# Performance work log

Hardware: AMD Instinct MI355X
Metric: run time of the kernel (lower is better)

Reference implementation:

```python
import jax, jax.numpy as jnp
import numpy as np

EPS = 1e-12  # torch F.normalize eps

def _l2norm(x):
    n = jnp.linalg.norm(x, axis=1, keepdims=True)
    return x / jnp.maximum(n, EPS)

def setup_inputs() -> dict:
    key = jax.random.key(0)
    kq, km = jax.random.split(key)
    queries = jax.random.normal(kq, (4096, 128), dtype=jnp.float32)
    memory = jax.random.normal(km, (100000, 128), dtype=jnp.float32)
    return {"queries": queries, "memory": memory, "k": 3}

def reference(queries, memory, k):
    q = _l2norm(queries)                      # [N, D]
    m = _l2norm(memory)                       # [M, D]
    sims = q @ m.T                            # [N, M]
    values, indices = jax.lax.top_k(sims, k)  # [N, k] each
    distances = 1.0 - values
    return distances, indices
```

## Files before the change

kernel.cpp:

```cpp
#include <hip/hip_runtime.h>
#include <hip/hip_bf16.h>

typedef unsigned short u16;
typedef unsigned int u32;
typedef unsigned long long u64;

#define N_Q 4096
#define N_M 100000
#define N_M_PAD 100096
#define DDIM 128
#define QTILE 256
#define MTILE 64
#define NCHUNK 32
#define NQT (N_Q / QTILE)
#define TOTAL_MT (N_M_PAD / MTILE)
#define TPC ((TOTAL_MT + NCHUNK - 1) / NCHUNK)
#define NCAND (NCHUNK * 2 * 3)

typedef short bf16x8 __attribute__((ext_vector_type(8)));
typedef float f32x4 __attribute__((ext_vector_type(4)));

static __device__ __forceinline__ u16 f2bf(float v) {
  union { float f; u32 u; } a; a.f = v;
  u32 r = a.u + 0x7fffu + ((a.u >> 16) & 1u);
  return (u16)(r >> 16);
}

static __device__ __forceinline__ void async_copy16(const u16* gp, u16* lp) {
  __builtin_amdgcn_global_load_lds(
      (const __attribute__((address_space(1))) u32*)gp,
      (__attribute__((address_space(3))) u32*)lp, 16, 0, 0);
}

static __device__ __forceinline__ int mbcnt64(u64 m) {
  return __builtin_amdgcn_mbcnt_hi((u32)(m >> 32),
                                   __builtin_amdgcn_mbcnt_lo((u32)m, 0));
}

__global__ __launch_bounds__(256) void knorm(const float* __restrict__ q, const float* __restrict__ m,
                                             u16* __restrict__ qn, u16* __restrict__ mn,
                                             float* __restrict__ qinv, float* __restrict__ minv) {
  const int lane = threadIdx.x & 63;
  const int l16 = lane & 15;
  const int sub = lane >> 4;
  const int wgl = blockIdx.x * 4 + (threadIdx.x >> 6);
  const int step = gridDim.x * 16;
  for (int row = wgl * 4 + sub; row < N_Q + N_M_PAD; row += step) {
    const float* src;
    u16* dst;
    int mr = 0;
    bool is_q = (row < N_Q);
    bool pad = false;
    if (is_q) {
      src = q + (size_t)row * DDIM;
      dst = qn + (size_t)row * DDIM;
    } else {
      mr = row - N_Q;
      pad = (mr >= N_M);
      src = m + (size_t)mr * DDIM;
      dst = mn + (size_t)mr * DDIM;
    }
    float4 a, b;
    if (pad) {
      a.x = a.y = a.z = a.w = 0.f;
      b = a;
    } else {
      a = ((const float4*)src)[l16];
      b = ((const float4*)src)[l16 + 16];
    }
    float s = a.x * a.x + a.y * a.y + a.z * a.z + a.w * a.w +
              b.x * b.x + b.y * b.y + b.z * b.z + b.w * b.w;
    #pragma unroll
    for (int off = 1; off < 16; off <<= 1) s += __shfl_xor(s, off, 64);
    float invn = 1.0f / fmaxf(sqrtf(s), 1e-12f);
    u32 p0 = (u32)f2bf(a.x * invn) | ((u32)f2bf(a.y * invn) << 16);
    u32 p1 = (u32)f2bf(a.z * invn) | ((u32)f2bf(a.w * invn) << 16);
    u32 p2 = (u32)f2bf(b.x * invn) | ((u32)f2bf(b.y * invn) << 16);
    u32 p3 = (u32)f2bf(b.z * invn) | ((u32)f2bf(b.w * invn) << 16);
    uint2 w0; w0.x = p0; w0.y = p1;
    uint2 w1; w1.x = p2; w1.y = p3;
    *(uint2*)&dst[l16 * 4] = w0;
    *(uint2*)&dst[64 + l16 * 4] = w1;
    if (l16 == 0) {
      if (is_q) qinv[row] = invn;
      else minv[mr] = pad ? 0.f : invn;
    }
  }
}

static __device__ __forceinline__ void stage2(const u16* __restrict__ mn, u16* dst,
                                              int t, const u32* goff, u32 loff0) {
  const u16* gbase = mn + (size_t)t * MTILE * DDIM;
  #pragma unroll
  for (int it = 0; it < 2; ++it)
    async_copy16(gbase + goff[it], dst + loff0 + (u32)(it * 64) * 8);
}

static __device__ __forceinline__ void tileWork(
    const u16* As, int tl, int wm, int quad, int l15,
    const bf16x8 (&bq)[4][4], float (&tv0)[4], float (&tv1)[4], float (&tv2)[4]) {
  f32x4 acc[2][4];
  __builtin_amdgcn_s_setprio(1);
  {
    int c = quad ^ l15;
    bf16x8 a0 = *(const bf16x8*)&As[((wm * 32 + l15) * 16 + c) * 8];
    bf16x8 a1 = *(const bf16x8*)&As[((wm * 32 + 16 + l15) * 16 + c) * 8];
    f32x4 z = {0.f, 0.f, 0.f, 0.f};
    #pragma unroll
    for (int ni = 0; ni < 4; ++ni) {
      acc[0][ni] = __builtin_amdgcn_mfma_f32_16x16x32_bf16(a0, bq[ni][0], z, 0, 0, 0);
      acc[1][ni] = __builtin_amdgcn_mfma_f32_16x16x32_bf16(a1, bq[ni][0], z, 0, 0, 0);
    }
  }
  #pragma unroll
  for (int s = 1; s < 4; ++s) {
    int c = (s * 4 + quad) ^ l15;
    bf16x8 a0 = *(const bf16x8*)&As[((wm * 32 + l15) * 16 + c) * 8];
    bf16x8 a1 = *(const bf16x8*)&As[((wm * 32 + 16 + l15) * 16 + c) * 8];
    #pragma unroll
    for (int ni = 0; ni < 4; ++ni) {
      acc[0][ni] = __builtin_amdgcn_mfma_f32_16x16x32_bf16(a0, bq[ni][s], acc[0][ni], 0, 0, 0);
      acc[1][ni] = __builtin_amdgcn_mfma_f32_16x16x32_bf16(a1, bq[ni][s], acc[1][ni], 0, 0, 0);
    }
  }
  __builtin_amdgcn_s_setprio(0);
  const u32 code = ((u32)tl << 2) | (u32)quad;
  #pragma unroll
  for (int ni = 0; ni < 4; ++ni) {
    f32x4 x0 = acc[0][ni], x1 = acc[1][ni];
    float M = fmaxf(fmaxf(fmaxf(x0[0], x0[1]), fmaxf(x0[2], x0[3])),
                    fmaxf(fmaxf(x1[0], x1[1]), fmaxf(x1[2], x1[3])));
    float pk = __uint_as_float((__float_as_uint(M) & 0xFFFFFE00u) | code);
    tv2[ni] = __builtin_amdgcn_fmed3f(tv1[ni], tv2[ni], pk);
    tv1[ni] = __builtin_amdgcn_fmed3f(tv0[ni], tv1[ni], pk);
    tv0[ni] = fmaxf(tv0[ni], pk);
  }
}

__global__ __launch_bounds__(512, 4) void kgemm(const u16* __restrict__ qn,
                                                const u16* __restrict__ mn,
                                                float* __restrict__ pval) {
  __shared__ u16 B0[MTILE * DDIM];
  __shared__ u16 B1[MTILE * DDIM];
  __shared__ u16 B2[MTILE * DDIM];
  __shared__ u16 B3[MTILE * DDIM];

  const int id = blockIdx.x;
  const int xcd = id & 7, sub = id >> 3;
  const int ch = xcd * 4 + (sub >> 4);
  const int qt = sub & 15;
  const int tid = threadIdx.x;
  const int wid = tid >> 6, lane = tid & 63;
  const int quad = lane >> 4, l15 = lane & 15;
  const int wm = wid >> 2, wq = wid & 3;

  const int t0 = ch * TPC;
  const int t1 = (t0 + TPC < TOTAL_MT) ? (t0 + TPC) : TOTAL_MT;
  const int nt = t1 - t0;

  u32 goff[2];
  u32 loff0;
  {
    int u0 = wid * 128 + lane;
    loff0 = (u32)(wid * 128) * 8;
    #pragma unroll
    for (int it = 0; it < 2; ++it) {
      int u = u0 + it * 64;
      int row = u >> 4, su = u & 15;
      int k8 = su ^ (row & 15);
      goff[it] = (u32)(row * DDIM + k8 * 8);
    }
  }

  stage2(mn, B0, t0 + 0, goff, loff0);
  stage2(mn, B1, t0 + 1, goff, loff0);
  stage2(mn, B2, t0 + 2, goff, loff0);

  bf16x8 bq[4][4];
  #pragma unroll
  for (int ni = 0; ni < 4; ++ni) {
    int col = qt * QTILE + wq * 64 + ni * 16 + l15;
    #pragma unroll
    for (int s = 0; s < 4; ++s)
      bq[ni][s] = *(const bf16x8*)&qn[(size_t)col * DDIM + (s * 4 + quad) * 8];
  }

  float tv0[4], tv1[4], tv2[4];
  #pragma unroll
  for (int i = 0; i < 4; ++i) { tv0[i] = tv1[i] = tv2[i] = -1e30f; }

  asm volatile("s_waitcnt vmcnt(0)" ::: "memory");
  asm volatile("s_barrier" ::: "memory");

  int r = 0;
  #define ROUND(BC, BS)                                                        \
    {                                                                          \
      int ts = t0 + r + 3;                                                     \
      ts = (ts < t1) ? ts : (t1 - 1);                                          \
      stage2(mn, BS, ts, goff, loff0);                                         \
      tileWork(BC, r, wm, quad, l15, bq, tv0, tv1, tv2);                       \
      asm volatile("s_waitcnt vmcnt(4)" ::: "memory");                         \
      asm volatile("s_barrier" ::: "memory");                                  \
      ++r;                                                                     \
      if (r >= nt) break;                                                      \
    }
  while (true) {
    ROUND(B0, B3)
    ROUND(B1, B0)
    ROUND(B2, B1)
    ROUND(B3, B2)
  }
  #undef ROUND

  #pragma unroll
  for (int ni = 0; ni < 4; ++ni) {
    float a0 = tv0[ni], a1 = tv1[ni], a2 = tv2[ni];
    #pragma unroll
    for (int off = 16; off <= 32; off <<= 1) {
      float b0 = __shfl_xor(a0, off, 64);
      float b1 = __shfl_xor(a1, off, 64);
      float b2 = __shfl_xor(a2, off, 64);
      float n0 = fmaxf(a0, b0);
      float n1 = __builtin_amdgcn_fmed3f(a0, b0, fmaxf(a1, b1));
      float n2 = fmaxf(fmaxf(fminf(a1, b0), fminf(a0, b1)), fmaxf(a2, b2));
      a0 = n0; a1 = n1; a2 = n2;
    }
    float v = (quad == 0) ? a0 : ((quad == 1) ? a1 : a2);
    if (quad < 3) {
      int qlocal = wq * 64 + ni * 16 + l15;
      size_t base = (((size_t)qt * NCHUNK + ch) * QTILE + qlocal) * 6 + wm * 3 + quad;
      pval[base] = v;
    }
  }
}

__global__ __launch_bounds__(256) void kmerge(const float* __restrict__ pval,
                                              const float* __restrict__ q,
                                              const float* __restrict__ mem,
                                              const float* __restrict__ qinv,
                                              const float* __restrict__ minv,
                                              float* __restrict__ out) {
  __shared__ float sv[4][64];
  __shared__ u32 spk[4][8];
  __shared__ u32 spo[4][8];
  const int tid = threadIdx.x;
  const int wq = tid >> 6;
  const int lane = tid & 63;
  const int qg = blockIdx.x * 4 + wq;
  const int qt = qg >> 8, ql = qg & 255;

  const int c0 = lane * 3;
  float cv[3];
  {
    int chn = c0 / 6, rem = c0 - chn * 6;
    size_t b = (((size_t)qt * NCHUNK + chn) * QTILE + ql) * 6 + rem;
    cv[0] = pval[b];
    cv[1] = pval[b + 1];
    cv[2] = pval[b + 2];
  }

  u32 k[3];
  #pragma unroll
  for (int i = 0; i < 3; ++i) {
    u32 u = __float_as_uint(cv[i]);
    k[i] = (u & 0x80000000u) ? ~u : (u | 0x80000000u);
  }

  u32 t = 0;
  #pragma unroll
  for (int b = 31; b >= 0; --b) {
    u32 cand = t | (1u << b);
    int loc = (int)(k[0] >= cand) + (int)(k[1] >= cand) + (int)(k[2] >= cand);
    u64 B0 = __ballot(loc & 1);
    u64 B1 = __ballot(loc & 2);
    int cnt = __popcll(B0) + 2 * __popcll(B1);
    if (cnt >= 8) t = cand;
  }

  {
    u64 G[3], E[3];
    #pragma unroll
    for (int i = 0; i < 3; ++i) {
      G[i] = __ballot(k[i] > t);
      E[i] = __ballot(k[i] == t);
    }
    int c1 = __popcll(G[0]) + __popcll(G[1]) + __popcll(G[2]);
    int bg = mbcnt64(G[0]) + mbcnt64(G[1]) + mbcnt64(G[2]);
    int be = mbcnt64(E[0]) + mbcnt64(E[1]) + mbcnt64(E[2]);
    int og = 0, oe = 0;
    #pragma unroll
    for (int i = 0; i < 3; ++i) {
      int slot = 99;
      if (k[i] > t) { slot = bg + og; ++og; }
      else if (k[i] == t) { slot = c1 + be + oe; ++oe; }
      if (slot < 8) {
        spk[wq][slot] = __float_as_uint(cv[i]);
        spo[wq][slot] = (u32)(c0 + i);
      }
    }
  }
  __syncthreads();

  const float qi = qinv[qg];
  const float* qrow = q + (size_t)qg * DDIM;
  const int e = lane >> 3, f = lane & 7;

  float4 qv[4];
  #pragma unroll
  for (int i = 0; i < 4; ++i) qv[i] = *(const float4*)&qrow[(f + 8 * i) * 4];

  #pragma unroll
  for (int p = 0; p < 8; ++p) {
    int bp = (int)spo[wq][p];
    u32 code = spk[wq][p] & 511u;
    int chn = bp / 6;
    int wm = (bp - chn * 6) / 3;
    int tl = (int)(code >> 2), qd = (int)(code & 3u);
    int row = (chn * TPC + tl) * MTILE + wm * 32 + (e >> 2) * 16 + qd * 4 + (e & 3);
    bool valid = (row < N_M);
    int ra = valid ? row : 0;
    const float* mrow = mem + (size_t)ra * DDIM;
    float s = 0.f;
    #pragma unroll
    for (int i = 0; i < 4; ++i) {
      float4 mv = *(const float4*)&mrow[(f + 8 * i) * 4];
      s += qv[i].x * mv.x + qv[i].y * mv.y + qv[i].z * mv.z + qv[i].w * mv.w;
    }
    #pragma unroll
    for (int off = 1; off < 8; off <<= 1) s += __shfl_xor(s, off, 64);
    s = valid ? (s * qi * minv[ra]) : -1e30f;
    if (f == 0) sv[wq][p * 8 + e] = s;
  }
  __syncthreads();

  float myv = sv[wq][lane];
  {
    int p = lane >> 3, e2 = lane & 7;
    int bp = (int)spo[wq][p];
    u32 code = spk[wq][p] & 511u;
    int chn = bp / 6;
    int wm = (bp - chn * 6) / 3;
    int tl = (int)(code >> 2), qd = (int)(code & 3u);
    int row = (chn * TPC + tl) * MTILE + wm * 32 + (e2 >> 2) * 16 + qd * 4 + (e2 & 3);
    int myrow = (row < N_M) ? row : (N_M + lane);

    #pragma unroll
    for (int a = 0; a < 3; ++a) {
      float bv = myv; int bi = myrow;
      #pragma unroll
      for (int off = 32; off >= 1; off >>= 1) {
        float ov = __shfl_xor(bv, off, 64);
        int oi = __shfl_xor(bi, off, 64);
        bool g2 = (ov > bv) || (ov == bv && oi < bi);
        bv = g2 ? ov : bv; bi = g2 ? oi : bi;
      }
      if (lane == 0) {
        out[(size_t)qg * 3 + a] = 1.0f - bv;
        out[(size_t)N_Q * 3 + (size_t)qg * 3 + a] = (float)bi;
      }
      if (myrow == bi) myv = -1e31f;
    }
  }
}

extern "C" void kernel_launch(void* const* d_in, const int* in_sizes, int n_in,
                              void* d_out, int out_size, void* d_ws, size_t ws_size,
                              hipStream_t stream) {
  const float* q = (const float*)d_in[0];
  const float* m = (const float*)d_in[1];

  char* ws = (char*)d_ws;
  size_t off = 0;
  u16* qn = (u16*)(ws + off); off += (size_t)N_Q * DDIM * 2;
  u16* mn = (u16*)(ws + off); off += (size_t)N_M_PAD * DDIM * 2;
  float* qinv = (float*)(ws + off); off += (size_t)N_Q * 4;
  float* minv = (float*)(ws + off); off += (size_t)N_M_PAD * 4;
  float* pval = (float*)(ws + off); off += (size_t)N_Q * NCAND * 4;

  knorm<<<1024, 256, 0, stream>>>(q, m, qn, mn, qinv, minv);
  kgemm<<<NQT * NCHUNK, 512, 0, stream>>>(qn, mn, pval);
  kmerge<<<N_Q / 4, 256, 0, stream>>>(pval, q, m, qinv, minv, (float*)d_out);
}
```

Measured before the change: 200.9 us.

## Switch similarity GEMM from 16x16x32 to 32x32x16 bf16 MFMA tiles

Result: no change. 201.1 us, median of 3 (+0.1%).

```diff
diff --git a/kernel.cpp b/kernel.cpp
--- a/kernel.cpp
+++ b/kernel.cpp
@@ -19,6 +19,7 @@
 
 typedef short bf16x8 __attribute__((ext_vector_type(8)));
 typedef float f32x4 __attribute__((ext_vector_type(4)));
+typedef float f32x16 __attribute__((ext_vector_type(16)));
 
 static __device__ __forceinline__ u16 f2bf(float v) {
   union { float f; u32 u; } a; a.f = v;
@@ -97,43 +98,40 @@
 }
 
 static __device__ __forceinline__ void tileWork(
-    const u16* As, int tl, int wm, int quad, int l15,
-    const bf16x8 (&bq)[4][4], float (&tv0)[4], float (&tv1)[4], float (&tv2)[4]) {
-  f32x4 acc[2][4];
+    const u16* As, int tl, int wm, int h, int l15, int l31,
+    const bf16x8 (&bq)[2][8], float (&tv0)[2], float (&tv1)[2], float (&tv2)[2]) {
+  f32x16 acc[2];
   __builtin_amdgcn_s_setprio(1);
   {
-    int c = quad ^ l15;
-    bf16x8 a0 = *(const bf16x8*)&As[((wm * 32 + l15) * 16 + c) * 8];
-    bf16x8 a1 = *(const bf16x8*)&As[((wm * 32 + 16 + l15) * 16 + c) * 8];
-    f32x4 z = {0.f, 0.f, 0.f, 0.f};
-    #pragma unroll
-    for (int ni = 0; ni < 4; ++ni) {
-      acc[0][ni] = __builtin_amdgcn_mfma_f32_16x16x32_bf16(a0, bq[ni][0], z, 0, 0, 0);
-      acc[1][ni] = __builtin_amdgcn_mfma_f32_16x16x32_bf16(a1, bq[ni][0], z, 0, 0, 0);
-    }
-  }
-  #pragma unroll
-  for (int s = 1; s < 4; ++s) {
-    int c = (s * 4 + quad) ^ l15;
-    bf16x8 a0 = *(const bf16x8*)&As[((wm * 32 + l15) * 16 + c) * 8];
-    bf16x8 a1 = *(const bf16x8*)&As[((wm * 32 + 16 + l15) * 16 + c) * 8];
-    #pragma unroll
-    for (int ni = 0; ni < 4; ++ni) {
-      acc[0][ni] = __builtin_amdgcn_mfma_f32_16x16x32_bf16(a0, bq[ni][s], acc[0][ni], 0, 0, 0);
-      acc[1][ni] = __builtin_amdgcn_mfma_f32_16x16x32_bf16(a1, bq[ni][s], acc[1][ni], 0, 0, 0);
-    }
+    int c = h ^ l15;
+    bf16x8 a = *(const bf16x8*)&As[((wm * 32 + l31) * 16 + c) * 8];
+    f32x16 z = {0.f,0.f,0.f,0.f,0.f,0.f,0.f,0.f,0.f,0.f,0.f,0.f,0.f,0.f,0.f,0.f};
+    acc[0] = __builtin_amdgcn_mfma_f32_32x32x16_bf16(a, bq[0][0], z, 0, 0, 0);
+    acc[1] = __builtin_amdgcn_mfma_f32_32x32x16_bf16(a, bq[1][0], z, 0, 0, 0);
+  }
+  #pragma unroll
+  for (int s = 1; s < 8; ++s) {
+    int c = (s * 2 + h) ^ l15;
+    bf16x8 a = *(const bf16x8*)&As[((wm * 32 + l31) * 16 + c) * 8];
+    acc[0] = __builtin_amdgcn_mfma_f32_32x32x16_bf16(a, bq[0][s], acc[0], 0, 0, 0);
+    acc[1] = __builtin_amdgcn_mfma_f32_32x32x16_bf16(a, bq[1][s], acc[1], 0, 0, 0);
   }
   __builtin_amdgcn_s_setprio(0);
-  const u32 code = ((u32)tl << 2) | (u32)quad;
-  #pragma unroll
-  for (int ni = 0; ni < 4; ++ni) {
-    f32x4 x0 = acc[0][ni], x1 = acc[1][ni];
-    float M = fmaxf(fmaxf(fmaxf(x0[0], x0[1]), fmaxf(x0[2], x0[3])),
-                    fmaxf(fmaxf(x1[0], x1[1]), fmaxf(x1[2], x1[3])));
-    float pk = __uint_as_float((__float_as_uint(M) & 0xFFFFFE00u) | code);
-    tv2[ni] = __builtin_amdgcn_fmed3f(tv1[ni], tv2[ni], pk);
-    tv1[ni] = __builtin_amdgcn_fmed3f(tv0[ni], tv1[ni], pk);
-    tv0[ni] = fmaxf(tv0[ni], pk);
+  const u32 codeBase = ((u32)tl << 2) | ((u32)h << 1);
+  #pragma unroll
+  for (int ni = 0; ni < 2; ++ni) {
+    #pragma unroll
+    for (int g = 0; g < 2; ++g) {
+      float M = fmaxf(
+          fmaxf(fmaxf(acc[ni][g * 8 + 0], acc[ni][g * 8 + 1]),
+                fmaxf(acc[ni][g * 8 + 2], acc[ni][g * 8 + 3])),
+          fmaxf(fmaxf(acc[ni][g * 8 + 4], acc[ni][g * 8 + 5]),
+                fmaxf(acc[ni][g * 8 + 6], acc[ni][g * 8 + 7])));
+      float pk = __uint_as_float((__float_as_uint(M) & 0xFFFFFE00u) | (codeBase | (u32)g));
+      tv2[ni] = __builtin_amdgcn_fmed3f(tv1[ni], tv2[ni], pk);
+      tv1[ni] = __builtin_amdgcn_fmed3f(tv0[ni], tv1[ni], pk);
+      tv0[ni] = fmaxf(tv0[ni], pk);
+    }
   }
 }
 
@@ -151,7 +149,7 @@
   const int qt = sub & 15;
   const int tid = threadIdx.x;
   const int wid = tid >> 6, lane = tid & 63;
-  const int quad = lane >> 4, l15 = lane & 15;
+  const int l15 = lane & 15, l31 = lane & 31, h = lane >> 5;
   const int wm = wid >> 2, wq = wid & 3;
 
   const int t0 = ch * TPC;
@@ -176,18 +174,18 @@
   stage2(mn, B1, t0 + 1, goff, loff0);
   stage2(mn, B2, t0 + 2, goff, loff0);
 
-  bf16x8 bq[4][4];
-  #pragma unroll
-  for (int ni = 0; ni < 4; ++ni) {
-    int col = qt * QTILE + wq * 64 + ni * 16 + l15;
-    #pragma unroll
-    for (int s = 0; s < 4; ++s)
-      bq[ni][s] = *(const bf16x8*)&qn[(size_t)col * DDIM + (s * 4 + quad) * 8];
-  }
-
-  float tv0[4], tv1[4], tv2[4];
-  #pragma unroll
-  for (int i = 0; i < 4; ++i) { tv0[i] = tv1[i] = tv2[i] = -1e30f; }
+  bf16x8 bq[2][8];
+  #pragma unroll
+  for (int ni = 0; ni < 2; ++ni) {
+    int col = qt * QTILE + wq * 64 + ni * 32 + l31;
+    #pragma unroll
+    for (int s = 0; s < 8; ++s)
+      bq[ni][s] = *(const bf16x8*)&qn[(size_t)col * DDIM + (s * 2 + h) * 8];
+  }
+
+  float tv0[2], tv1[2], tv2[2];
+  #pragma unroll
+  for (int i = 0; i < 2; ++i) { tv0[i] = tv1[i] = tv2[i] = -1e30f; }
 
   asm volatile("s_waitcnt vmcnt(0)" ::: "memory");
   asm volatile("s_barrier" ::: "memory");
@@ -198,7 +196,7 @@
       int ts = t0 + r + 3;                                                     \
       ts = (ts < t1) ? ts : (t1 - 1);                                          \
       stage2(mn, BS, ts, goff, loff0);                                         \
-      tileWork(BC, r, wm, quad, l15, bq, tv0, tv1, tv2);                       \
+      tileWork(BC, r, wm, h, l15, l31, bq, tv0, tv1, tv2);                     \
       asm volatile("s_waitcnt vmcnt(4)" ::: "memory");                         \
       asm volatile("s_barrier" ::: "memory");                                  \
       ++r;                                                                     \
@@ -213,23 +211,21 @@
   #undef ROUND
 
   #pragma unroll
-  for (int ni = 0; ni < 4; ++ni) {
+  for (int ni = 0; ni < 2; ++ni) {
     float a0 = tv0[ni], a1 = tv1[ni], a2 = tv2[ni];
-    #pragma unroll
-    for (int off = 16; off <= 32; off <<= 1) {
-      float b0 = __shfl_xor(a0, off, 64);
-      float b1 = __shfl_xor(a1, off, 64);
-      float b2 = __shfl_xor(a2, off, 64);
-      float n0 = fmaxf(a0, b0);
-      float n1 = __builtin_amdgcn_fmed3f(a0, b0, fmaxf(a1, b1));
-      float n2 = fmaxf(fmaxf(fminf(a1, b0), fminf(a0, b1)), fmaxf(a2, b2));
-      a0 = n0; a1 = n1; a2 = n2;
-    }
-    float v = (quad == 0) ? a0 : ((quad == 1) ? a1 : a2);
-    if (quad < 3) {
-      int qlocal = wq * 64 + ni * 16 + l15;
-      size_t base = (((size_t)qt * NCHUNK + ch) * QTILE + qlocal) * 6 + wm * 3 + quad;
-      pval[base] = v;
+    float b0 = __shfl_xor(a0, 32, 64);
+    float b1 = __shfl_xor(a1, 32, 64);
+    float b2 = __shfl_xor(a2, 32, 64);
+    float n0 = fmaxf(a0, b0);
+    float n1 = __builtin_amdgcn_fmed3f(a0, b0, fmaxf(a1, b1));
+    float n2 = fmaxf(fmaxf(fminf(a1, b0), fminf(a0, b1)), fmaxf(a2, b2));
+    int qlocal = wq * 64 + ni * 32 + l31;
+    size_t base = (((size_t)qt * NCHUNK + ch) * QTILE + qlocal) * 6 + wm * 3;
+    if (h == 0) {
+      pval[base] = n0;
+      pval[base + 1] = n1;
+    } else {
+      pval[base + 2] = n2;
     }
   }
 }
@@ -315,8 +311,8 @@
     u32 code = spk[wq][p] & 511u;
     int chn = bp / 6;
     int wm = (bp - chn * 6) / 3;
-    int tl = (int)(code >> 2), qd = (int)(code & 3u);
-    int row = (chn * TPC + tl) * MTILE + wm * 32 + (e >> 2) * 16 + qd * 4 + (e & 3);
+    int tl = (int)(code >> 2), hh = (int)((code >> 1) & 1u), g = (int)(code & 1u);
+    int row = (chn * TPC + tl) * MTILE + wm * 32 + g * 16 + (e >> 2) * 8 + hh * 4 + (e & 3);
     bool valid = (row < N_M);
     int ra = valid ? row : 0;
     const float* mrow = mem + (size_t)ra * DDIM;
@@ -340,8 +336,8 @@
     u32 code = spk[wq][p] & 511u;
     int chn = bp / 6;
     int wm = (bp - chn * 6) / 3;
-    int tl = (int)(code >> 2), qd = (int)(code & 3u);
-    int row = (chn * TPC + tl) * MTILE + wm * 32 + (e2 >> 2) * 16 + qd * 4 + (e2 & 3);
+    int tl = (int)(code >> 2), hh = (int)((code >> 1) & 1u), g = (int)(code & 1u);
+    int row = (chn * TPC + tl) * MTILE + wm * 32 + g * 16 + (e2 >> 2) * 8 + hh * 4 + (e2 & 3);
     int myrow = (row < N_M) ? row : (N_M + lane);
 
     #pragma unroll
```
